# Performance work log

Measured on AMD Instinct MI355X. Metric: run time of the kernel, lower is better.

The kernel has to match this reference:

```python
import jax, jax.numpy as jnp
import numpy as np

T, B, D_IN, E, HA, HB, D_OUT = 64, 64, 4096, 128, 128, 128, 4096


def setup_inputs() -> dict:
    key = jax.random.key(0)
    ks = jax.random.split(key, 18)

    def u(k, shape, fan):
        b = 1.0 / np.sqrt(fan)
        return jax.random.uniform(k, shape, jnp.float32, -b, b)

    return {
        "x": jax.random.uniform(ks[0], (T, B, D_IN), jnp.float32),
        "W_emb": u(ks[1], (E, D_IN), D_IN), "b_emb": u(ks[2], (E,), D_IN),
        "W_ih_a": u(ks[3], (3 * HA, E), HA), "W_hh_a": u(ks[4], (3 * HA, HA), HA),
        "b_ih_a": u(ks[5], (3 * HA,), HA), "b_hh_a": u(ks[6], (3 * HA,), HA),
        "W_ih_b": u(ks[7], (3 * HB, E), HB), "W_hh_b": u(ks[8], (3 * HB, HB), HB),
        "b_ih_b": u(ks[9], (3 * HB,), HB), "b_hh_b": u(ks[10], (3 * HB,), HB),
        "w_alpha": u(ks[11], (1, HA), HA), "b_alpha": u(ks[12], (1,), HA),
        "W_beta": u(ks[13], (E, HB), HB), "b_beta": u(ks[14], (E,), HB),
        "W_out": u(ks[15], (D_OUT, E), E), "b_out": u(ks[16], (D_OUT,), E),
    }


def _gru_states(emb, W_ih, W_hh, b_ih, b_hh):
    # For every query position i, run a GRU over the reversed prefix
    # emb[i], emb[i-1], ..., emb[0] from h0 = 0. All T queries are batched.
    # Returns hs[s, i, b, h] = hidden of query i after step s (input emb[i-s]).
    Tlen, Bsz, _ = emb.shape
    H = W_hh.shape[1]
    i_arr = jnp.arange(Tlen)

    def step(h, s):
        idx = jnp.clip(i_arr - s, 0, Tlen - 1)          # (T,) input index per query
        xs = emb[idx]                                    # (T, B, E)
        gi = xs @ W_ih.T + b_ih                          # (T, B, 3H)
        gh = h @ W_hh.T + b_hh
        i_r, i_z, i_n = jnp.split(gi, 3, axis=-1)
        h_r, h_z, h_n = jnp.split(gh, 3, axis=-1)
        r = jax.nn.sigmoid(i_r + h_r)
        z = jax.nn.sigmoid(i_z + h_z)
        n = jnp.tanh(i_n + r * h_n)
        h_new = (1.0 - z) * n + z * h
        return h_new, h_new

    h0 = jnp.zeros((Tlen, Bsz, H), emb.dtype)
    _, hs = jax.lax.scan(step, h0, jnp.arange(Tlen))
    return hs  # (S, T, B, H)


def _retain_forward(x, W_emb, b_emb, W_ih_a, W_hh_a, b_ih_a, b_hh_a,
                    W_ih_b, W_hh_b, b_ih_b, b_hh_b, w_alpha, b_alpha,
                    W_beta, b_beta, W_out, b_out):
    Tlen = x.shape[0]
    emb = x @ W_emb.T + b_emb                            # (T, B, E)

    hs_a = _gru_states(emb, W_ih_a, W_hh_a, b_ih_a, b_hh_a)  # (S, T, B, HA)
    hs_b = _gru_states(emb, W_ih_b, W_hh_b, b_ih_b, b_hh_b)  # (S, T, B, HB)

    i_arr = jnp.arange(Tlen)
    # reverse_h[i, j] = hidden after processing emb[i..j] (reverse order) = hs[i - j, i]
    rev = jnp.clip(i_arr[:, None] - i_arr[None, :], 0, Tlen - 1)  # (T, T)
    rh_a = hs_a[rev, i_arr[:, None]] * 0.5               # (T, T, B, HA)
    rh_b = hs_b[rev, i_arr[:, None]] * 0.5               # (T, T, B, HB)

    mask = (i_arr[None, :] <= i_arr[:, None])            # (T, T): j <= i valid
    logits = jnp.einsum('ijbh,h->ijb', rh_a, w_alpha[0]) + b_alpha[0]
    logits = jnp.where(mask[:, :, None], logits, -1e9)
    alpha = jax.nn.softmax(logits, axis=1)               # softmax over prefix steps j
    alpha = alpha * mask[:, :, None].astype(alpha.dtype)

    beta = jnp.tanh(rh_b @ W_beta.T + b_beta)            # (T, T, B, E)

    # c[i] = mean_{j<=i} alpha[i,j] * beta[i,j] * emb[j]
    c = jnp.einsum('ijb,ijbe->ibe', alpha, beta * emb[None, :, :, :])
    counts = jnp.arange(1, Tlen + 1, dtype=c.dtype)[:, None, None]
    c = c / counts

    return jax.nn.sigmoid(c @ W_out.T + b_out)           # (T, B, D_OUT)


def reference(x, W_emb, b_emb, W_ih_a, W_hh_a, b_ih_a, b_hh_a,
              W_ih_b, W_hh_b, b_ih_b, b_hh_b, w_alpha, b_alpha,
              W_beta, b_beta, W_out, b_out):
    return _retain_forward(x, W_emb, b_emb, W_ih_a, W_hh_a, b_ih_a, b_hh_a,
                           W_ih_b, W_hh_b, b_ih_b, b_hh_b, w_alpha, b_alpha,
                           W_beta, b_beta, W_out, b_out)
```

## Files before the change

kernel.cpp:

```cpp
#include <hip/hip_runtime.h>
#include <hip/hip_bf16.h>


typedef __attribute__((ext_vector_type(8))) short short8;
typedef __attribute__((ext_vector_type(4))) float f32x4;
typedef _Float16 half8 __attribute__((ext_vector_type(8)));

#define MFMA16(a, b, c) __builtin_amdgcn_mfma_f32_16x16x32_bf16((a), (b), (c), 0, 0, 0)

#define LOG2E 1.4426950408889634f
#define TLOG2E 2.8853900817779268f

__device__ __forceinline__ unsigned pkbf(float a, float b) {
  __hip_bfloat162 t = __float22bfloat162_rn(float2{a, b});
  return *reinterpret_cast<unsigned*>(&t);
}
__device__ __forceinline__ float ex2(float x) { return __builtin_amdgcn_exp2f(x); }
__device__ __forceinline__ float rcpa(float x) { return __builtin_amdgcn_rcpf(x); }
__device__ __forceinline__ float tanh2(float y) {
  float e = ex2(-fmaxf(y, -126.0f));
  return (1.0f - e) * rcpa(1.0f + e);
}

#define OFF_GI3    16777216u
#define OFF_WEMB   27262976u
#define OFF_WOUT   28311552u
#define OFF_WHHA   29360128u
#define OFF_WHHB   29458432u
#define OFF_WIH    29556736u
#define OFF_WBETA  29753344u

__global__ void k_prep(const float* W_emb, const float* W_out,
                       const float* W_hh_a, const float* W_hh_b,
                       const float* W_ih_a, const float* W_ih_b,
                       const float* W_beta,
                       unsigned* wemb, unsigned* wout,
                       unsigned* whha, unsigned* whhb,
                       unsigned* wih, unsigned* wbeta) {
  const unsigned total = 630784u;
  for (unsigned idx = blockIdx.x * 256u + threadIdx.x; idx < total;
       idx += gridDim.x * 256u) {
    unsigned i = idx;
    if (i < 262144u) { float2 v = ((const float2*)W_emb)[i]; wemb[i] = pkbf(v.x, v.y); continue; }
    i -= 262144u;
    if (i < 262144u) { float2 v = ((const float2*)W_out)[i]; wout[i] = pkbf(v.x, v.y); continue; }
    i -= 262144u;
    if (i < 24576u) {
      float2 v = ((const float2*)W_hh_a)[i];
      const float sc = ((i >> 13) == 2u) ? TLOG2E : LOG2E;
      whha[i] = pkbf(sc * v.x, sc * v.y); continue;
    }
    i -= 24576u;
    if (i < 24576u) {
      float2 v = ((const float2*)W_hh_b)[i];
      const float sc = ((i >> 13) == 2u) ? TLOG2E : LOG2E;
      whhb[i] = pkbf(sc * v.x, sc * v.y); continue;
    }
    i -= 24576u;
    if (i < 24576u) {
      float2 v = ((const float2*)W_ih_a)[i];
      const float sc = ((i >> 13) == 2u) ? TLOG2E : LOG2E;
      wih[i] = pkbf(sc * v.x, sc * v.y); continue;
    }
    i -= 24576u;
    if (i < 24576u) {
      float2 v = ((const float2*)W_ih_b)[i];
      const float sc = ((i >> 13) == 2u) ? TLOG2E : LOG2E;
      wih[24576u + i] = pkbf(sc * v.x, sc * v.y); continue;
    }
    i -= 24576u;
    { float2 v = ((const float2*)W_beta)[i]; wbeta[i] = pkbf(LOG2E * v.x, LOG2E * v.y); }
  }
}

__global__ __launch_bounds__(512) void k_front(const float* __restrict__ x,
                                               const unsigned short* __restrict__ wemb,
                                               const unsigned short* __restrict__ wih,
                                               const float* __restrict__ b_emb,
                                               const float* __restrict__ b_ih_a,
                                               const float* __restrict__ b_ih_b,
                                               const float* __restrict__ b_hh_a,
                                               const float* __restrict__ b_hh_b,
                                               _Float16* __restrict__ gih) {
  const int tid = threadIdx.x, w = tid >> 6, lane = tid & 63, q = lane >> 4, ln = lane & 15;
  const int m0 = blockIdx.x * 16;

  __shared__ float part[8][16][132];
  __shared__ unsigned short embs[16][136];

  const f32x4 zero = {0.f, 0.f, 0.f, 0.f};

  {
    f32x4 acc[8];
#pragma unroll
    for (int nt = 0; nt < 8; ++nt) acc[nt] = zero;

    const float* xp = x + (size_t)(m0 + ln) * 4096 + w * 512 + q * 8;
    const unsigned short* wp = wemb + (size_t)ln * 4096 + w * 512 + q * 8;

#pragma unroll 4
    for (int kk = 0; kk < 16; ++kk) {
      const int ko = kk * 32;
      float4 u0 = *(const float4*)(xp + ko);
      float4 u1 = *(const float4*)(xp + ko + 4);
      union { short8 v; unsigned u[4]; } a0;
      a0.u[0] = pkbf(u0.x, u0.y); a0.u[1] = pkbf(u0.z, u0.w);
      a0.u[2] = pkbf(u1.x, u1.y); a0.u[3] = pkbf(u1.z, u1.w);
#pragma unroll
      for (int nt = 0; nt < 8; ++nt) {
        short8 b = *(const short8*)(wp + (size_t)(nt * 16) * 4096 + ko);
        acc[nt] = MFMA16(a0.v, b, acc[nt]);
      }
    }
#pragma unroll
    for (int nt = 0; nt < 8; ++nt)
#pragma unroll
      for (int r = 0; r < 4; ++r)
        part[w][q * 4 + r][nt * 16 + ln] = acc[nt][r];
  }
  __syncthreads();

  {
    const int row = tid & 15, col0 = (tid >> 4) * 4;
    f32x4 s = *(const f32x4*)(b_emb + col0);
#pragma unroll
    for (int ww = 0; ww < 8; ++ww) {
      const f32x4 v = *(const f32x4*)&part[ww][row][col0];
      s[0] += v[0]; s[1] += v[1]; s[2] += v[2]; s[3] += v[3];
    }
    _Float16* g6 = gih + (size_t)(m0 + row) * 1024 + 6;
#pragma unroll
    for (int j = 0; j < 4; ++j) g6[(size_t)(col0 + j) * 8] = (_Float16)s[j];
    *(unsigned*)&embs[row][col0]     = pkbf(s[0], s[1]);
    *(unsigned*)&embs[row][col0 + 2] = pkbf(s[2], s[3]);
  }
  __syncthreads();

  {
    short8 af[4];
#pragma unroll
    for (int kc = 0; kc < 4; ++kc)
      af[kc] = *(const short8*)&embs[ln][kc * 32 + q * 8];

    const int nb = w * 96;
    f32x4 acg[6];
#pragma unroll
    for (int nt = 0; nt < 6; ++nt) acg[nt] = zero;

#pragma unroll
    for (int kc = 0; kc < 4; ++kc) {
      const int ko = kc * 32 + q * 8;
#pragma unroll
      for (int nt = 0; nt < 6; ++nt) {
        short8 b = *(const short8*)(wih + (size_t)(nb + nt * 16 + ln) * 128 + ko);
        acg[nt] = MFMA16(af[kc], b, acg[nt]);
      }
    }
#pragma unroll
    for (int nt = 0; nt < 6; ++nt) {
      const int g = nb + nt * 16 + ln;
      const int gg = g >> 7, kout = g & 127;
      float bias;
      if (g < 384) bias = b_ih_a[g] + ((gg < 2) ? b_hh_a[g] : 0.0f);
      else {
        const int g2 = g - 384;
        bias = b_ih_b[g2] + ((gg < 5) ? b_hh_b[g2] : 0.0f);
      }
      bias *= (gg == 2 || gg == 5) ? TLOG2E : LOG2E;
#pragma unroll
      for (int r = 0; r < 4; ++r)
        gih[(size_t)(m0 + q * 4 + r) * 1024 + kout * 8 + gg] = (_Float16)(acg[nt][r] + bias);
    }
  }
}

__global__ __launch_bounds__(512) __attribute__((amdgpu_waves_per_eu(2, 2)))
void k_recur(const _Float16* __restrict__ gih,
             const unsigned short* __restrict__ whha, const unsigned short* __restrict__ whhb,
             const unsigned short* __restrict__ wbeta,
             const float* __restrict__ b_hh_a, const float* __restrict__ b_hh_b,
             const float* __restrict__ b_beta, const float* __restrict__ b_alpha,
             const float* __restrict__ w_alpha,
             const unsigned short* __restrict__ wout,
             const float* __restrict__ b_out,
             float* __restrict__ out) {
  const int tid = threadIdx.x, w = tid >> 6, lane = tid & 63, q = lane >> 4, ln = lane & 15;
  const int p = blockIdx.x >> 3, btile = blockIdx.x & 7;
  const int i1 = p, i2 = 63 - p;
  const int kout = w * 16 + ln;

  __shared__ unsigned short hA[2][16 * 136], hB[2][16 * 136];

  for (int idx = tid; idx < 16 * 136; idx += 512) { hA[0][idx] = 0; hB[0][idx] = 0; }

  const int iq = (q < 2) ? i1 : i2;
  const _Float16* gp[4];
#pragma unroll
  for (int r = 0; r < 4; ++r) {
    const int b = btile * 8 + (q & 1) * 4 + r;
    gp[r] = gih + (size_t)(iq * 64 + b) * 1024 + kout * 8;
  }

  short8 fra[3][4], frb[3][4];
#pragma unroll
  for (int g = 0; g < 3; ++g) {
    const unsigned short* ba = whha + (size_t)(g * 128 + kout) * 128;
    const unsigned short* bb = whhb + (size_t)(g * 128 + kout) * 128;
#pragma unroll
    for (int kc = 0; kc < 4; ++kc) {
      fra[g][kc] = *(const short8*)(ba + kc * 32 + q * 8);
      frb[g][kc] = *(const short8*)(bb + kc * 32 + q * 8);
    }
  }
#pragma unroll
  for (int g = 0; g < 3; ++g)
#pragma unroll
    for (int kc = 0; kc < 4; ++kc) {
      asm volatile("" : "+a"(fra[g][kc]));
      asm volatile("" : "+a"(frb[g][kc]));
    }

  short8 fbe[4];
#pragma unroll
  for (int kc = 0; kc < 4; ++kc) {
    fbe[kc] = *(const short8*)(wbeta + (size_t)(w * 16 + ln) * 128 + kc * 32 + q * 8);
    asm volatile("" : "+a"(fbe[kc]));
  }

  short8 fal[4];
#pragma unroll
  for (int kc = 0; kc < 4; ++kc) {
    float4 w0 = *(const float4*)(w_alpha + kc * 32 + q * 8);
    float4 w1 = *(const float4*)(w_alpha + kc * 32 + q * 8 + 4);
    union { short8 v; unsigned u[4]; } t;
    t.u[0] = pkbf(0.5f * LOG2E * w0.x, 0.5f * LOG2E * w0.y);
    t.u[1] = pkbf(0.5f * LOG2E * w0.z, 0.5f * LOG2E * w0.w);
    t.u[2] = pkbf(0.5f * LOG2E * w1.x, 0.5f * LOG2E * w1.y);
    t.u[3] = pkbf(0.5f * LOG2E * w1.z, 0.5f * LOG2E * w1.w);
    fal[kc] = t.v;
    asm volatile("" : "+a"(fal[kc]));
  }

  const float bhnA = TLOG2E * b_hh_a[256 + kout];
  const float bhnB = TLOG2E * b_hh_b[256 + kout];
  const float bbet = TLOG2E * b_beta[kout];
  const float bal = LOG2E * b_alpha[0];

  float hRA[4], hRB[4], cac[4], lreg[4], embp[4];
#pragma unroll
  for (int r = 0; r < 4; ++r) { hRA[r] = 0.f; hRB[r] = 0.f; cac[r] = 0.f; lreg[r] = 0.f; embp[r] = 0.f; }

  const f32x4 zero = {0.f, 0.f, 0.f, 0.f};
  int jj = iq;
  half8 ngv[4];
#pragma unroll
  for (int r = 0; r < 4; ++r) ngv[r] = *(const half8*)gp[r];

  __syncthreads();

  for (int s = 0; s <= i2; ++s) {
    const int rb = s & 1, wb = rb ^ 1;

    half8 gv[4];
#pragma unroll
    for (int r = 0; r < 4; ++r) gv[r] = ngv[r];

    short8 haf[4], hbf[4];
#pragma unroll
    for (int kc = 0; kc < 4; ++kc) {
      haf[kc] = *(const short8*)(hA[rb] + ln * 136 + kc * 32 + q * 8);
      hbf[kc] = *(const short8*)(hB[rb] + ln * 136 + kc * 32 + q * 8);
    }

    f32x4 accA[3] = {zero, zero, zero}, accB[3] = {zero, zero, zero};
    f32x4 accV = zero, accL = zero;
#pragma unroll
    for (int kc = 0; kc < 4; ++kc) {
#pragma unroll
      for (int g = 0; g < 3; ++g) {
        accA[g] = MFMA16(haf[kc], fra[g][kc], accA[g]);
        accB[g] = MFMA16(hbf[kc], frb[g][kc], accB[g]);
      }
      accV = MFMA16(hbf[kc], fbe[kc], accV);
      accL = MFMA16(haf[kc], fal[kc], accL);
    }

    const bool act = ((unsigned)(s - 1) <= (unsigned)iq);
#pragma unroll
    for (int r = 0; r < 4; ++r) {
      const float logit = accL[r] + bal;
      const float pp = act ? ex2(logit) : 0.0f;
      lreg[r] += pp;
      const float beta = tanh2(accV[r] + bbet);
      cac[r] += pp * beta * embp[r];
    }

#pragma unroll
    for (int r = 0; r < 4; ++r) {
      const int rowoff = (q * 4 + r) * 136 + kout;

      const float erA = ex2(-((float)gv[r][0] + accA[0][r]));
      const float rA = rcpa(1.0f + erA);
      const float tA = (float)gv[r][2] + rA * (accA[2][r] + bhnA);
      const float enA = ex2(-fmaxf(tA, -62.0f));
      const float ezA = ex2(-fmaxf((float)gv[r][1] + accA[1][r], -62.0f));
      const float apnA = 1.0f + enA, apzA = 1.0f + ezA;
      const float numA = fmaf(hRA[r], apnA, ezA * (1.0f - enA));
      const float hnA = numA * rcpa(apnA * apzA);
      hRA[r] = hnA;
      hA[wb][rowoff] = (unsigned short)pkbf(hnA, hnA);

      const float erB = ex2(-((float)gv[r][3] + accB[0][r]));
      const float rB = rcpa(1.0f + erB);
      const float tB = (float)gv[r][5] + rB * (accB[2][r] + bhnB);
      const float enB = ex2(-fmaxf(tB, -62.0f));
      const float ezB = ex2(-fmaxf((float)gv[r][4] + accB[1][r], -62.0f));
      const float apnB = 1.0f + enB, apzB = 1.0f + ezB;
      const float numB = fmaf(hRB[r], apnB, ezB * (1.0f - enB));
      const float hnB = numB * rcpa(apnB * apzB);
      hRB[r] = hnB;
      hB[wb][rowoff] = (unsigned short)pkbf(hnB, hnB);

      embp[r] = (float)gv[r][6];
    }

    if (jj > 0) {
      --jj;
#pragma unroll
      for (int r = 0; r < 4; ++r) gp[r] -= 65536;
    }
#pragma unroll
    for (int r = 0; r < 4; ++r) ngv[r] = *(const half8*)gp[r];

    asm volatile("s_waitcnt lgkmcnt(0)\n\ts_barrier" ::: "memory");
  }

  {
    const int rb2 = (i2 + 1) & 1;
    short8 haf[4], hbf[4];
#pragma unroll
    for (int kc = 0; kc < 4; ++kc) {
      haf[kc] = *(const short8*)(hA[rb2] + ln * 136 + kc * 32 + q * 8);
      hbf[kc] = *(const short8*)(hB[rb2] + ln * 136 + kc * 32 + q * 8);
    }
    f32x4 accV = zero, accL = zero;
#pragma unroll
    for (int kc = 0; kc < 4; ++kc) {
      accV = MFMA16(hbf[kc], fbe[kc], accV);
      accL = MFMA16(haf[kc], fal[kc], accL);
    }
    const bool act = (iq == i2);
#pragma unroll
    for (int r = 0; r < 4; ++r) {
      const float logit = accL[r] + bal;
      const float pp = act ? ex2(logit) : 0.0f;
      lreg[r] += pp;
      const float beta = tanh2(accV[r] + bbet);
      cac[r] += pp * beta * embp[r];
    }
  }

  __syncthreads();
  {
    const int crow0 = (q >= 2 ? 8 : 0) + (q & 1) * 4;
#pragma unroll
    for (int r = 0; r < 4; ++r) {
      const float val = cac[r] * rcpa(lreg[r] * (float)(iq + 1));
      hA[0][(crow0 + r) * 136 + kout] = (unsigned short)pkbf(val, val);
    }
  }
  __syncthreads();

  {
    short8 cb[4];
#pragma unroll
    for (int kc = 0; kc < 4; ++kc)
      cb[kc] = *(const short8*)(hA[0] + ln * 136 + kc * 32 + q * 8);

    const int m_glob = ((ln >= 8) ? i2 : i1) * 64 + btile * 8 + (ln & 7);
    float* orow = out + (size_t)m_glob * 4096;
    const int nb0 = w * 512;

    for (int nt = 0; nt < 32; ++nt) {
      const int n16 = nb0 + nt * 16;
      f32x4 acc = zero;
#pragma unroll
      for (int kc = 0; kc < 4; ++kc) {
        short8 a = *(const short8*)(wout + (size_t)(n16 + ln) * 128 + kc * 32 + q * 8);
        acc = MFMA16(a, cb[kc], acc);
      }
      const int n0 = n16 + q * 4;
      const float4 bo = *(const float4*)(b_out + n0);
      float4 o;
      o.x = rcpa(1.0f + ex2(-LOG2E * (acc[0] + bo.x)));
      o.y = rcpa(1.0f + ex2(-LOG2E * (acc[1] + bo.y)));
      o.z = rcpa(1.0f + ex2(-LOG2E * (acc[2] + bo.z)));
      o.w = rcpa(1.0f + ex2(-LOG2E * (acc[3] + bo.w)));
      *(float4*)(orow + n0) = o;
    }
  }
}

extern "C" void kernel_launch(void* const* d_in, const int* in_sizes, int n_in,
                              void* d_out, int out_size, void* d_ws, size_t ws_size,
                              hipStream_t stream) {
  const float* x      = (const float*)d_in[0];
  const float* W_emb  = (const float*)d_in[1];
  const float* b_emb  = (const float*)d_in[2];
  const float* W_ih_a = (const float*)d_in[3];
  const float* W_hh_a = (const float*)d_in[4];
  const float* b_ih_a = (const float*)d_in[5];
  const float* b_hh_a = (const float*)d_in[6];
  const float* W_ih_b = (const float*)d_in[7];
  const float* W_hh_b = (const float*)d_in[8];
  const float* b_ih_b = (const float*)d_in[9];
  const float* b_hh_b = (const float*)d_in[10];
  const float* w_alpha = (const float*)d_in[11];
  const float* b_alpha = (const float*)d_in[12];
  const float* W_beta = (const float*)d_in[13];
  const float* b_beta = (const float*)d_in[14];
  const float* W_out  = (const float*)d_in[15];
  const float* b_out  = (const float*)d_in[16];
  float* out = (float*)d_out;

  char* ws = (char*)d_ws;
  _Float16*       gih    = (_Float16*)(ws + OFF_GI3);
  unsigned*       wemb   = (unsigned*)(ws + OFF_WEMB);
  unsigned*       wout   = (unsigned*)(ws + OFF_WOUT);
  unsigned*       whha   = (unsigned*)(ws + OFF_WHHA);
  unsigned*       whhb   = (unsigned*)(ws + OFF_WHHB);
  unsigned*       wih    = (unsigned*)(ws + OFF_WIH);
  unsigned*       wbeta  = (unsigned*)(ws + OFF_WBETA);

  k_prep<<<1024, 256, 0, stream>>>(W_emb, W_out, W_hh_a, W_hh_b, W_ih_a, W_ih_b,
                                   W_beta, wemb, wout, whha, whhb, wih, wbeta);
  k_front<<<256, 512, 0, stream>>>(x, (const unsigned short*)wemb,
                                   (const unsigned short*)wih, b_emb,
                                   b_ih_a, b_ih_b, b_hh_a, b_hh_b, gih);
  k_recur<<<256, 512, 0, stream>>>(gih, (const unsigned short*)whha,
                                   (const unsigned short*)whhb, (const unsigned short*)wbeta,
                                   b_hh_a, b_hh_b, b_beta, b_alpha, w_alpha,
                                   (const unsigned short*)wout, b_out, out);
}
```

Baseline: 326.6 us.

## Split output projection into separate kernel and stage gih stores via LDS

Moves the final W_out projection and sigmoid out of the serial recurrence kernel into a new k_out kernel with 2048 blocks. k_recur now writes the bf16 context vectors to a workspace buffer, so the 64 MB output write is spread over many more waves instead of 256 blocks. k_front also software-prefetches the next x chunk in its embedding loop, and stages the gih tile in shared memory so it can be written with coalesced 16-byte stores instead of scattered 2-byte stores. The cost is one extra launch and a small round trip through global memory for the context vectors.

```diff
diff --git a/kernel.cpp b/kernel.cpp
--- a/kernel.cpp
+++ b/kernel.cpp
@@ -23,6 +23,7 @@
 }
 
 #define OFF_GI3    16777216u
+#define OFF_CBF    26214400u
 #define OFF_WEMB   27262976u
 #define OFF_WOUT   28311552u
 #define OFF_WHHA   29360128u
@@ -98,19 +99,23 @@
     const float* xp = x + (size_t)(m0 + ln) * 4096 + w * 512 + q * 8;
     const unsigned short* wp = wemb + (size_t)ln * 4096 + w * 512 + q * 8;
 
-#pragma unroll 4
+    float4 u0 = *(const float4*)(xp);
+    float4 u1 = *(const float4*)(xp + 4);
     for (int kk = 0; kk < 16; ++kk) {
-      const int ko = kk * 32;
-      float4 u0 = *(const float4*)(xp + ko);
-      float4 u1 = *(const float4*)(xp + ko + 4);
+      float4 n0, n1;
+      if (kk < 15) {
+        n0 = *(const float4*)(xp + kk * 32 + 32);
+        n1 = *(const float4*)(xp + kk * 32 + 36);
+      }
       union { short8 v; unsigned u[4]; } a0;
       a0.u[0] = pkbf(u0.x, u0.y); a0.u[1] = pkbf(u0.z, u0.w);
       a0.u[2] = pkbf(u1.x, u1.y); a0.u[3] = pkbf(u1.z, u1.w);
 #pragma unroll
       for (int nt = 0; nt < 8; ++nt) {
-        short8 b = *(const short8*)(wp + (size_t)(nt * 16) * 4096 + ko);
+        short8 b = *(const short8*)(wp + (size_t)(nt * 16) * 4096 + kk * 32);
         acc[nt] = MFMA16(a0.v, b, acc[nt]);
       }
+      u0 = n0; u1 = n1;
     }
 #pragma unroll
     for (int nt = 0; nt < 8; ++nt)
@@ -120,21 +125,26 @@
   }
   __syncthreads();
 
+  const int rrow = tid & 15, col0 = (tid >> 4) * 4;
+  f32x4 sred = *(const f32x4*)(b_emb + col0);
   {
-    const int row = tid & 15, col0 = (tid >> 4) * 4;
-    f32x4 s = *(const f32x4*)(b_emb + col0);
 #pragma unroll
     for (int ww = 0; ww < 8; ++ww) {
-      const f32x4 v = *(const f32x4*)&part[ww][row][col0];
-      s[0] += v[0]; s[1] += v[1]; s[2] += v[2]; s[3] += v[3];
-    }
-    _Float16* g6 = gih + (size_t)(m0 + row) * 1024 + 6;
-#pragma unroll
-    for (int j = 0; j < 4; ++j) g6[(size_t)(col0 + j) * 8] = (_Float16)s[j];
-    *(unsigned*)&embs[row][col0]     = pkbf(s[0], s[1]);
-    *(unsigned*)&embs[row][col0 + 2] = pkbf(s[2], s[3]);
+      const f32x4 v = *(const f32x4*)&part[ww][rrow][col0];
+      sred[0] += v[0]; sred[1] += v[1]; sred[2] += v[2]; sred[3] += v[3];
+    }
+    *(unsigned*)&embs[rrow][col0]     = pkbf(sred[0], sred[1]);
+    *(unsigned*)&embs[rrow][col0 + 2] = pkbf(sred[2], sred[3]);
   }
   __syncthreads();
+
+  _Float16* stage = (_Float16*)&part[0][0][0];
+
+#pragma unroll
+  for (int j = 0; j < 4; ++j) {
+    stage[rrow * 1032 + (col0 + j) * 8 + 6] = (_Float16)sred[j];
+    stage[rrow * 1032 + (col0 + j) * 8 + 7] = (_Float16)0.0f;
+  }
 
   {
     short8 af[4];
@@ -169,7 +179,18 @@
       bias *= (gg == 2 || gg == 5) ? TLOG2E : LOG2E;
 #pragma unroll
       for (int r = 0; r < 4; ++r)
-        gih[(size_t)(m0 + q * 4 + r) * 1024 + kout * 8 + gg] = (_Float16)(acg[nt][r] + bias);
+        stage[(q * 4 + r) * 1032 + kout * 8 + gg] = (_Float16)(acg[nt][r] + bias);
+    }
+  }
+  __syncthreads();
+
+  {
+    const int row2 = tid >> 5, seg = tid & 31;
+#pragma unroll
+    for (int k = 0; k < 4; ++k) {
+      const int off = (seg + k * 32) * 8;
+      *(short8*)(gih + (size_t)(m0 + row2) * 1024 + off) =
+          *(const short8*)(stage + row2 * 1032 + off);
     }
   }
 }
@@ -181,9 +202,7 @@
              const float* __restrict__ b_hh_a, const float* __restrict__ b_hh_b,
              const float* __restrict__ b_beta, const float* __restrict__ b_alpha,
              const float* __restrict__ w_alpha,
-             const unsigned short* __restrict__ wout,
-             const float* __restrict__ b_out,
-             float* __restrict__ out) {
+             unsigned short* __restrict__ cbf) {
   const int tid = threadIdx.x, w = tid >> 6, lane = tid & 63, q = lane >> 4, ln = lane & 15;
   const int p = blockIdx.x >> 3, btile = blockIdx.x & 7;
   const int i1 = p, i2 = 63 - p;
@@ -360,44 +379,48 @@
     }
   }
 
-  __syncthreads();
-  {
-    const int crow0 = (q >= 2 ? 8 : 0) + (q & 1) * 4;
-#pragma unroll
-    for (int r = 0; r < 4; ++r) {
-      const float val = cac[r] * rcpa(lreg[r] * (float)(iq + 1));
-      hA[0][(crow0 + r) * 136 + kout] = (unsigned short)pkbf(val, val);
-    }
-  }
-  __syncthreads();
-
-  {
-    short8 cb[4];
-#pragma unroll
-    for (int kc = 0; kc < 4; ++kc)
-      cb[kc] = *(const short8*)(hA[0] + ln * 136 + kc * 32 + q * 8);
-
-    const int m_glob = ((ln >= 8) ? i2 : i1) * 64 + btile * 8 + (ln & 7);
-    float* orow = out + (size_t)m_glob * 4096;
-    const int nb0 = w * 512;
-
-    for (int nt = 0; nt < 32; ++nt) {
-      const int n16 = nb0 + nt * 16;
-      f32x4 acc = zero;
-#pragma unroll
-      for (int kc = 0; kc < 4; ++kc) {
-        short8 a = *(const short8*)(wout + (size_t)(n16 + ln) * 128 + kc * 32 + q * 8);
-        acc = MFMA16(a, cb[kc], acc);
-      }
-      const int n0 = n16 + q * 4;
-      const float4 bo = *(const float4*)(b_out + n0);
-      float4 o;
-      o.x = rcpa(1.0f + ex2(-LOG2E * (acc[0] + bo.x)));
-      o.y = rcpa(1.0f + ex2(-LOG2E * (acc[1] + bo.y)));
-      o.z = rcpa(1.0f + ex2(-LOG2E * (acc[2] + bo.z)));
-      o.w = rcpa(1.0f + ex2(-LOG2E * (acc[3] + bo.w)));
-      *(float4*)(orow + n0) = o;
-    }
+#pragma unroll
+  for (int r = 0; r < 4; ++r) {
+    const int b = btile * 8 + (q & 1) * 4 + r;
+    const float val = cac[r] * rcpa(lreg[r] * (float)(iq + 1));
+    cbf[(size_t)(iq * 64 + b) * 128 + kout] = (unsigned short)pkbf(val, val);
+  }
+}
+
+__global__ __launch_bounds__(256) void k_out(const unsigned short* __restrict__ cbf,
+                                             const unsigned short* __restrict__ wout,
+                                             const float* __restrict__ b_out,
+                                             float* __restrict__ out) {
+  const int mt = blockIdx.x >> 3, nq = blockIdx.x & 7;
+  const int w = threadIdx.x >> 6, lane = threadIdx.x & 63, q = lane >> 4, ln = lane & 15;
+  const int m0 = mt * 16;
+  const f32x4 zero = {0.f, 0.f, 0.f, 0.f};
+
+  short8 cb[4];
+#pragma unroll
+  for (int kc = 0; kc < 4; ++kc)
+    cb[kc] = *(const short8*)(cbf + (size_t)(m0 + ln) * 128 + kc * 32 + q * 8);
+
+  float* orow = out + (size_t)(m0 + ln) * 4096;
+  const int nb0 = nq * 512 + w * 128;
+
+#pragma unroll
+  for (int nt = 0; nt < 8; ++nt) {
+    const int n16 = nb0 + nt * 16;
+    f32x4 acc = zero;
+#pragma unroll
+    for (int kc = 0; kc < 4; ++kc) {
+      short8 a = *(const short8*)(wout + (size_t)(n16 + ln) * 128 + kc * 32 + q * 8);
+      acc = MFMA16(a, cb[kc], acc);
+    }
+    const int n0 = n16 + q * 4;
+    const float4 bo = *(const float4*)(b_out + n0);
+    float4 o;
+    o.x = rcpa(1.0f + ex2(-LOG2E * (acc[0] + bo.x)));
+    o.y = rcpa(1.0f + ex2(-LOG2E * (acc[1] + bo.y)));
+    o.z = rcpa(1.0f + ex2(-LOG2E * (acc[2] + bo.z)));
+    o.w = rcpa(1.0f + ex2(-LOG2E * (acc[3] + bo.w)));
+    *(float4*)(orow + n0) = o;
   }
 }
 
@@ -425,6 +448,7 @@
 
   char* ws = (char*)d_ws;
   _Float16*       gih    = (_Float16*)(ws + OFF_GI3);
+  unsigned short* cbf    = (unsigned short*)(ws + OFF_CBF);
   unsigned*       wemb   = (unsigned*)(ws + OFF_WEMB);
   unsigned*       wout   = (unsigned*)(ws + OFF_WOUT);
   unsigned*       whha   = (unsigned*)(ws + OFF_WHHA);
@@ -439,6 +463,6 @@
                                    b_ih_a, b_ih_b, b_hh_a, b_hh_b, gih);
   k_recur<<<256, 512, 0, stream>>>(gih, (const unsigned short*)whha,
                                    (const unsigned short*)whhb, (const unsigned short*)wbeta,
-                                   b_hh_a, b_hh_b, b_beta, b_alpha, w_alpha,
-                                   (const unsigned short*)wout, b_out, out);
-}
+                                   b_hh_a, b_hh_b, b_beta, b_alpha, w_alpha, cbf);
+  k_out<<<2048, 256, 0, stream>>>(cbf, (const unsigned short*)wout, b_out, out);
+}
```

Result: slower. 335.9 us (+2.9%).

## Fuse prep, front, and recurrence kernels into one cooperative kernel with grid syncs

Applied to the files above, without the earlier changes.

Merges the three launches (weight conversion, embedding/input-gate GEMM, recurrence) into a single cooperative kernel separated by grid-wide syncs. This removes two kernel launch gaps and their tail effects. The input-gate output is now staged in shared memory and written to global memory with coalesced 16-byte stores instead of scattered 2-byte stores. The cost is grid-sync overhead, larger combined LDS use, and the recurrence phase now running under the register limits of the fused kernel, which could lower occupancy or cause spills.

```diff
diff --git a/kernel.cpp b/kernel.cpp
--- a/kernel.cpp
+++ b/kernel.cpp
@@ -1,5 +1,8 @@
 #include <hip/hip_runtime.h>
 #include <hip/hip_bf16.h>
+#include <hip/hip_cooperative_groups.h>
+
+namespace cg = cooperative_groups;
 
 
 typedef __attribute__((ext_vector_type(8))) short short8;
@@ -30,166 +33,185 @@
 #define OFF_WIH    29556736u
 #define OFF_WBETA  29753344u
 
-__global__ void k_prep(const float* W_emb, const float* W_out,
-                       const float* W_hh_a, const float* W_hh_b,
-                       const float* W_ih_a, const float* W_ih_b,
-                       const float* W_beta,
-                       unsigned* wemb, unsigned* wout,
-                       unsigned* whha, unsigned* whhb,
-                       unsigned* wih, unsigned* wbeta) {
-  const unsigned total = 630784u;
-  for (unsigned idx = blockIdx.x * 256u + threadIdx.x; idx < total;
-       idx += gridDim.x * 256u) {
-    unsigned i = idx;
-    if (i < 262144u) { float2 v = ((const float2*)W_emb)[i]; wemb[i] = pkbf(v.x, v.y); continue; }
-    i -= 262144u;
-    if (i < 262144u) { float2 v = ((const float2*)W_out)[i]; wout[i] = pkbf(v.x, v.y); continue; }
-    i -= 262144u;
-    if (i < 24576u) {
-      float2 v = ((const float2*)W_hh_a)[i];
-      const float sc = ((i >> 13) == 2u) ? TLOG2E : LOG2E;
-      whha[i] = pkbf(sc * v.x, sc * v.y); continue;
-    }
-    i -= 24576u;
-    if (i < 24576u) {
-      float2 v = ((const float2*)W_hh_b)[i];
-      const float sc = ((i >> 13) == 2u) ? TLOG2E : LOG2E;
-      whhb[i] = pkbf(sc * v.x, sc * v.y); continue;
-    }
-    i -= 24576u;
-    if (i < 24576u) {
-      float2 v = ((const float2*)W_ih_a)[i];
-      const float sc = ((i >> 13) == 2u) ? TLOG2E : LOG2E;
-      wih[i] = pkbf(sc * v.x, sc * v.y); continue;
-    }
-    i -= 24576u;
-    if (i < 24576u) {
-      float2 v = ((const float2*)W_ih_b)[i];
-      const float sc = ((i >> 13) == 2u) ? TLOG2E : LOG2E;
-      wih[24576u + i] = pkbf(sc * v.x, sc * v.y); continue;
-    }
-    i -= 24576u;
-    { float2 v = ((const float2*)W_beta)[i]; wbeta[i] = pkbf(LOG2E * v.x, LOG2E * v.y); }
-  }
-}
-
-__global__ __launch_bounds__(512) void k_front(const float* __restrict__ x,
-                                               const unsigned short* __restrict__ wemb,
-                                               const unsigned short* __restrict__ wih,
-                                               const float* __restrict__ b_emb,
-                                               const float* __restrict__ b_ih_a,
-                                               const float* __restrict__ b_ih_b,
-                                               const float* __restrict__ b_hh_a,
-                                               const float* __restrict__ b_hh_b,
-                                               _Float16* __restrict__ gih) {
+__global__ __launch_bounds__(512) __attribute__((amdgpu_waves_per_eu(2, 2)))
+void k_mega(const float* __restrict__ x,
+            const float* __restrict__ W_emb, const float* __restrict__ b_emb,
+            const float* __restrict__ W_ih_a, const float* __restrict__ W_hh_a,
+            const float* __restrict__ b_ih_a, const float* __restrict__ b_hh_a,
+            const float* __restrict__ W_ih_b, const float* __restrict__ W_hh_b,
+            const float* __restrict__ b_ih_b, const float* __restrict__ b_hh_b,
+            const float* __restrict__ w_alpha, const float* __restrict__ b_alpha,
+            const float* __restrict__ W_beta, const float* __restrict__ b_beta,
+            const float* __restrict__ W_out, const float* __restrict__ b_out,
+            float* __restrict__ out, char* __restrict__ ws) {
   const int tid = threadIdx.x, w = tid >> 6, lane = tid & 63, q = lane >> 4, ln = lane & 15;
-  const int m0 = blockIdx.x * 16;
+
+  unsigned*       wembp  = (unsigned*)(ws + OFF_WEMB);
+  unsigned*       woutp  = (unsigned*)(ws + OFF_WOUT);
+  unsigned*       whhap  = (unsigned*)(ws + OFF_WHHA);
+  unsigned*       whhbp  = (unsigned*)(ws + OFF_WHHB);
+  unsigned*       wihp   = (unsigned*)(ws + OFF_WIH);
+  unsigned*       wbetap = (unsigned*)(ws + OFF_WBETA);
+  _Float16*       gih    = (_Float16*)(ws + OFF_GI3);
 
   __shared__ float part[8][16][132];
   __shared__ unsigned short embs[16][136];
+  __shared__ unsigned short hA[2][16 * 136], hB[2][16 * 136];
 
   const f32x4 zero = {0.f, 0.f, 0.f, 0.f};
 
   {
-    f32x4 acc[8];
-#pragma unroll
-    for (int nt = 0; nt < 8; ++nt) acc[nt] = zero;
-
-    const float* xp = x + (size_t)(m0 + ln) * 4096 + w * 512 + q * 8;
-    const unsigned short* wp = wemb + (size_t)ln * 4096 + w * 512 + q * 8;
+    const unsigned total = 630784u;
+    for (unsigned idx = blockIdx.x * 512u + tid; idx < total; idx += 131072u) {
+      unsigned i = idx;
+      if (i < 262144u) { float2 v = ((const float2*)W_emb)[i]; wembp[i] = pkbf(v.x, v.y); continue; }
+      i -= 262144u;
+      if (i < 262144u) { float2 v = ((const float2*)W_out)[i]; woutp[i] = pkbf(v.x, v.y); continue; }
+      i -= 262144u;
+      if (i < 24576u) {
+        float2 v = ((const float2*)W_hh_a)[i];
+        const float sc = ((i >> 13) == 2u) ? TLOG2E : LOG2E;
+        whhap[i] = pkbf(sc * v.x, sc * v.y); continue;
+      }
+      i -= 24576u;
+      if (i < 24576u) {
+        float2 v = ((const float2*)W_hh_b)[i];
+        const float sc = ((i >> 13) == 2u) ? TLOG2E : LOG2E;
+        whhbp[i] = pkbf(sc * v.x, sc * v.y); continue;
+      }
+      i -= 24576u;
+      if (i < 24576u) {
+        float2 v = ((const float2*)W_ih_a)[i];
+        const float sc = ((i >> 13) == 2u) ? TLOG2E : LOG2E;
+        wihp[i] = pkbf(sc * v.x, sc * v.y); continue;
+      }
+      i -= 24576u;
+      if (i < 24576u) {
+        float2 v = ((const float2*)W_ih_b)[i];
+        const float sc = ((i >> 13) == 2u) ? TLOG2E : LOG2E;
+        wihp[24576u + i] = pkbf(sc * v.x, sc * v.y); continue;
+      }
+      i -= 24576u;
+      { float2 v = ((const float2*)W_beta)[i]; wbetap[i] = pkbf(LOG2E * v.x, LOG2E * v.y); }
+    }
+  }
+  __threadfence();
+  cg::this_grid().sync();
+
+  {
+    const unsigned short* wemb = (const unsigned short*)wembp;
+    const unsigned short* wih = (const unsigned short*)wihp;
+    const int m0 = blockIdx.x * 16;
+
+    {
+      f32x4 acc[8];
+#pragma unroll
+      for (int nt = 0; nt < 8; ++nt) acc[nt] = zero;
+
+      const float* xp = x + (size_t)(m0 + ln) * 4096 + w * 512 + q * 8;
+      const unsigned short* wp = wemb + (size_t)ln * 4096 + w * 512 + q * 8;
 
 #pragma unroll 4
-    for (int kk = 0; kk < 16; ++kk) {
-      const int ko = kk * 32;
-      float4 u0 = *(const float4*)(xp + ko);
-      float4 u1 = *(const float4*)(xp + ko + 4);
-      union { short8 v; unsigned u[4]; } a0;
-      a0.u[0] = pkbf(u0.x, u0.y); a0.u[1] = pkbf(u0.z, u0.w);
-      a0.u[2] = pkbf(u1.x, u1.y); a0.u[3] = pkbf(u1.z, u1.w);
-#pragma unroll
-      for (int nt = 0; nt < 8; ++nt) {
-        short8 b = *(const short8*)(wp + (size_t)(nt * 16) * 4096 + ko);
-        acc[nt] = MFMA16(a0.v, b, acc[nt]);
-      }
-    }
-#pragma unroll
-    for (int nt = 0; nt < 8; ++nt)
-#pragma unroll
-      for (int r = 0; r < 4; ++r)
-        part[w][q * 4 + r][nt * 16 + ln] = acc[nt][r];
-  }
-  __syncthreads();
-
-  {
-    const int row = tid & 15, col0 = (tid >> 4) * 4;
-    f32x4 s = *(const f32x4*)(b_emb + col0);
-#pragma unroll
-    for (int ww = 0; ww < 8; ++ww) {
-      const f32x4 v = *(const f32x4*)&part[ww][row][col0];
-      s[0] += v[0]; s[1] += v[1]; s[2] += v[2]; s[3] += v[3];
-    }
-    _Float16* g6 = gih + (size_t)(m0 + row) * 1024 + 6;
-#pragma unroll
-    for (int j = 0; j < 4; ++j) g6[(size_t)(col0 + j) * 8] = (_Float16)s[j];
-    *(unsigned*)&embs[row][col0]     = pkbf(s[0], s[1]);
-    *(unsigned*)&embs[row][col0 + 2] = pkbf(s[2], s[3]);
-  }
-  __syncthreads();
-
-  {
-    short8 af[4];
-#pragma unroll
-    for (int kc = 0; kc < 4; ++kc)
-      af[kc] = *(const short8*)&embs[ln][kc * 32 + q * 8];
-
-    const int nb = w * 96;
-    f32x4 acg[6];
-#pragma unroll
-    for (int nt = 0; nt < 6; ++nt) acg[nt] = zero;
-
-#pragma unroll
-    for (int kc = 0; kc < 4; ++kc) {
-      const int ko = kc * 32 + q * 8;
+      for (int kk = 0; kk < 16; ++kk) {
+        const int ko = kk * 32;
+        float4 u0 = *(const float4*)(xp + ko);
+        float4 u1 = *(const float4*)(xp + ko + 4);
+        union { short8 v; unsigned u[4]; } a0;
+        a0.u[0] = pkbf(u0.x, u0.y); a0.u[1] = pkbf(u0.z, u0.w);
+        a0.u[2] = pkbf(u1.x, u1.y); a0.u[3] = pkbf(u1.z, u1.w);
+#pragma unroll
+        for (int nt = 0; nt < 8; ++nt) {
+          short8 b = *(const short8*)(wp + (size_t)(nt * 16) * 4096 + ko);
+          acc[nt] = MFMA16(a0.v, b, acc[nt]);
+        }
+      }
+#pragma unroll
+      for (int nt = 0; nt < 8; ++nt)
+#pragma unroll
+        for (int r = 0; r < 4; ++r)
+          part[w][q * 4 + r][nt * 16 + ln] = acc[nt][r];
+    }
+    __syncthreads();
+
+    const int rrow = tid & 15, col0 = (tid >> 4) * 4;
+    f32x4 sred = *(const f32x4*)(b_emb + col0);
+    {
+#pragma unroll
+      for (int ww = 0; ww < 8; ++ww) {
+        const f32x4 v = *(const f32x4*)&part[ww][rrow][col0];
+        sred[0] += v[0]; sred[1] += v[1]; sred[2] += v[2]; sred[3] += v[3];
+      }
+      *(unsigned*)&embs[rrow][col0]     = pkbf(sred[0], sred[1]);
+      *(unsigned*)&embs[rrow][col0 + 2] = pkbf(sred[2], sred[3]);
+    }
+    __syncthreads();
+
+    _Float16* stage = (_Float16*)&part[0][0][0];
+#pragma unroll
+    for (int j = 0; j < 4; ++j) {
+      stage[rrow * 1032 + (col0 + j) * 8 + 6] = (_Float16)sred[j];
+      stage[rrow * 1032 + (col0 + j) * 8 + 7] = (_Float16)0.0f;
+    }
+
+    {
+      short8 af[4];
+#pragma unroll
+      for (int kc = 0; kc < 4; ++kc)
+        af[kc] = *(const short8*)&embs[ln][kc * 32 + q * 8];
+
+      const int nb = w * 96;
+      f32x4 acg[6];
+#pragma unroll
+      for (int nt = 0; nt < 6; ++nt) acg[nt] = zero;
+
+#pragma unroll
+      for (int kc = 0; kc < 4; ++kc) {
+        const int ko = kc * 32 + q * 8;
+#pragma unroll
+        for (int nt = 0; nt < 6; ++nt) {
+          short8 b = *(const short8*)(wih + (size_t)(nb + nt * 16 + ln) * 128 + ko);
+          acg[nt] = MFMA16(af[kc], b, acg[nt]);
+        }
+      }
 #pragma unroll
       for (int nt = 0; nt < 6; ++nt) {
-        short8 b = *(const short8*)(wih + (size_t)(nb + nt * 16 + ln) * 128 + ko);
-        acg[nt] = MFMA16(af[kc], b, acg[nt]);
-      }
-    }
-#pragma unroll
-    for (int nt = 0; nt < 6; ++nt) {
-      const int g = nb + nt * 16 + ln;
-      const int gg = g >> 7, kout = g & 127;
-      float bias;
-      if (g < 384) bias = b_ih_a[g] + ((gg < 2) ? b_hh_a[g] : 0.0f);
-      else {
-        const int g2 = g - 384;
-        bias = b_ih_b[g2] + ((gg < 5) ? b_hh_b[g2] : 0.0f);
-      }
-      bias *= (gg == 2 || gg == 5) ? TLOG2E : LOG2E;
-#pragma unroll
-      for (int r = 0; r < 4; ++r)
-        gih[(size_t)(m0 + q * 4 + r) * 1024 + kout * 8 + gg] = (_Float16)(acg[nt][r] + bias);
-    }
-  }
-}
-
-__global__ __launch_bounds__(512) __attribute__((amdgpu_waves_per_eu(2, 2)))
-void k_recur(const _Float16* __restrict__ gih,
-             const unsigned short* __restrict__ whha, const unsigned short* __restrict__ whhb,
-             const unsigned short* __restrict__ wbeta,
-             const float* __restrict__ b_hh_a, const float* __restrict__ b_hh_b,
-             const float* __restrict__ b_beta, const float* __restrict__ b_alpha,
-             const float* __restrict__ w_alpha,
-             const unsigned short* __restrict__ wout,
-             const float* __restrict__ b_out,
-             float* __restrict__ out) {
-  const int tid = threadIdx.x, w = tid >> 6, lane = tid & 63, q = lane >> 4, ln = lane & 15;
+        const int g = nb + nt * 16 + ln;
+        const int gg = g >> 7, kout2 = g & 127;
+        float bias;
+        if (g < 384) bias = b_ih_a[g] + ((gg < 2) ? b_hh_a[g] : 0.0f);
+        else {
+          const int g2 = g - 384;
+          bias = b_ih_b[g2] + ((gg < 5) ? b_hh_b[g2] : 0.0f);
+        }
+        bias *= (gg == 2 || gg == 5) ? TLOG2E : LOG2E;
+#pragma unroll
+        for (int r = 0; r < 4; ++r)
+          stage[(q * 4 + r) * 1032 + kout2 * 8 + gg] = (_Float16)(acg[nt][r] + bias);
+      }
+    }
+    __syncthreads();
+
+    {
+      const int row2 = tid >> 5, seg = tid & 31;
+#pragma unroll
+      for (int k = 0; k < 4; ++k) {
+        const int off = (seg + k * 32) * 8;
+        *(short8*)(gih + (size_t)(m0 + row2) * 1024 + off) =
+            *(const short8*)(stage + row2 * 1032 + off);
+      }
+    }
+  }
+  __threadfence();
+  cg::this_grid().sync();
+
+  const unsigned short* whha = (const unsigned short*)whhap;
+  const unsigned short* whhb = (const unsigned short*)whhbp;
+  const unsigned short* wbeta = (const unsigned short*)wbetap;
+  const unsigned short* wout = (const unsigned short*)woutp;
+
   const int p = blockIdx.x >> 3, btile = blockIdx.x & 7;
   const int i1 = p, i2 = 63 - p;
   const int kout = w * 16 + ln;
-
-  __shared__ unsigned short hA[2][16 * 136], hB[2][16 * 136];
 
   for (int idx = tid; idx < 16 * 136; idx += 512) { hA[0][idx] = 0; hB[0][idx] = 0; }
 
@@ -250,7 +272,6 @@
 #pragma unroll
   for (int r = 0; r < 4; ++r) { hRA[r] = 0.f; hRB[r] = 0.f; cac[r] = 0.f; lreg[r] = 0.f; embp[r] = 0.f; }
 
-  const f32x4 zero = {0.f, 0.f, 0.f, 0.f};
   int jj = iq;
   half8 ngv[4];
 #pragma unroll
@@ -422,23 +443,15 @@
   const float* W_out  = (const float*)d_in[15];
   const float* b_out  = (const float*)d_in[16];
   float* out = (float*)d_out;
-
   char* ws = (char*)d_ws;
-  _Float16*       gih    = (_Float16*)(ws + OFF_GI3);
-  unsigned*       wemb   = (unsigned*)(ws + OFF_WEMB);
-  unsigned*       wout   = (unsigned*)(ws + OFF_WOUT);
-  unsigned*       whha   = (unsigned*)(ws + OFF_WHHA);
-  unsigned*       whhb   = (unsigned*)(ws + OFF_WHHB);
-  unsigned*       wih    = (unsigned*)(ws + OFF_WIH);
-  unsigned*       wbeta  = (unsigned*)(ws + OFF_WBETA);
-
-  k_prep<<<1024, 256, 0, stream>>>(W_emb, W_out, W_hh_a, W_hh_b, W_ih_a, W_ih_b,
-                                   W_beta, wemb, wout, whha, whhb, wih, wbeta);
-  k_front<<<256, 512, 0, stream>>>(x, (const unsigned short*)wemb,
-                                   (const unsigned short*)wih, b_emb,
-                                   b_ih_a, b_ih_b, b_hh_a, b_hh_b, gih);
-  k_recur<<<256, 512, 0, stream>>>(gih, (const unsigned short*)whha,
-                                   (const unsigned short*)whhb, (const unsigned short*)wbeta,
-                                   b_hh_a, b_hh_b, b_beta, b_alpha, w_alpha,
-                                   (const unsigned short*)wout, b_out, out);
+
+  void* args[] = {
+      (void*)&x, (void*)&W_emb, (void*)&b_emb, (void*)&W_ih_a, (void*)&W_hh_a,
+      (void*)&b_ih_a, (void*)&b_hh_a, (void*)&W_ih_b, (void*)&W_hh_b,
+      (void*)&b_ih_b, (void*)&b_hh_b, (void*)&w_alpha, (void*)&b_alpha,
+      (void*)&W_beta, (void*)&b_beta, (void*)&W_out, (void*)&b_out,
+      (void*)&out, (void*)&ws};
+
+  hipLaunchCooperativeKernel((const void*)k_mega, dim3(256), dim3(512), args, 0,
+                             stream);
 }
```

Result: slower. 503.6 us (+54.2%).
